# Optimization experiments

Hardware: AMD Instinct MI355X
Metric: run time of the kernel (lower is better)

Reference implementation:

```python
import jax, jax.numpy as jnp
import numpy as np

EPS = 1e-5
DOWNSAMPLE = 0.5


def setup_inputs() -> dict:
    key = jax.random.key(0)
    k1, k2, k3 = jax.random.split(key, 3)
    B, C, H, W = 32, 256, 128, 128
    x = jax.random.normal(k1, (B, C, H, W), dtype=jnp.float32)
    # 1x1 conv: weight [3, C], bias [3]
    conv_w = jax.random.normal(k2, (3, C), dtype=jnp.float32) / np.sqrt(C).astype(np.float32)
    conv_b = jax.random.normal(k3, (3,), dtype=jnp.float32) * 0.01
    return {"x": x, "conv_w": conv_w, "conv_b": conv_b}


def reference(x, conv_w, conv_b):
    B, C, H, W = x.shape
    dh = int(round(H * DOWNSAMPLE))
    dw = int(round(W * DOWNSAMPLE))

    # 1x1 conv producing 3 channels: 2 offset + 1 attention logit
    oa = jnp.einsum('bchw,oc->bohw', x, conv_w) + conv_b[None, :, None, None]
    offset = oa[:, :2]                      # [B,2,H,W]
    attention = jnp.exp(oa[:, 2:3])         # [B,1,H,W]

    # normalized destination coordinates = base grid + offset, clamped
    gy = jnp.broadcast_to((jnp.arange(H, dtype=x.dtype) / H)[:, None], (H, W))
    gx = jnp.broadcast_to((jnp.arange(W, dtype=x.dtype) / W)[None, :], (H, W))
    base = jnp.stack([gy, gx])              # [2,H,W]
    dest = jnp.clip(base[None] + offset, 0.0, 1.0 - EPS)
    dy = jnp.floor(dest[:, 0] * dh)
    dx = jnp.floor(dest[:, 1] * dw)
    cell = (dy * dw + dx).astype(jnp.int32)  # [B,H,W] spatial cell index

    # full flat destination index over (batch, channel, cell)
    b_off = jnp.arange(B, dtype=jnp.int32)[:, None, None, None] * (C * dh * dw)
    c_off = jnp.arange(C, dtype=jnp.int32)[None, :, None, None] * (dh * dw)
    destination = cell[:, None] + b_off + c_off  # [B,C,H,W]

    # scatter-add attention-weighted features
    xw = (x * attention).reshape(-1)
    feat = jax.ops.segment_sum(xw, destination.reshape(-1), num_segments=B * C * dh * dw)

    # scatter-add attention per (batch, cell) for normalization
    a_idx = cell + jnp.arange(B, dtype=jnp.int32)[:, None, None] * (dh * dw)
    att_sum = jax.ops.segment_sum(attention.reshape(-1), a_idx.reshape(-1), num_segments=B * dh * dw) + EPS

    out = feat.reshape(B, C, dh, dw) / att_sum.reshape(B, 1, dh, dw)
    return (out, offset, destination)
```

## Files before the change

### kernel.cpp

```cpp
#include <hip/hip_runtime.h>
#include <math.h>

#define NB 32
#define NC 256
#define NH 128
#define NW 128
#define NDH 64
#define NDW 64
#define NHW (NH * NW)
#define NCELLS (NDH * NDW)
#define OUT0_N (NB * NC * NCELLS)
#define OUT1_BASE OUT0_N
#define OUT1_N (NB * 2 * NHW)
#define OUT2_BASE (OUT1_BASE + OUT1_N)

#define EPSF 1e-5f

typedef unsigned short u16;
typedef unsigned int   u32;

#define WS_CELLS   ((size_t)0)
#define WS_ATTBF   (WS_CELLS + (size_t)NB*NHW*2)
#define WS_ECOMB   (WS_ATTBF + (size_t)NB*NHW*2)
#define WS_IASUM   (WS_ECOMB + (size_t)NB*NHW*4)

__device__ __forceinline__ u16 f32_to_bf16_rn(float f) {
    const u32 u = __float_as_uint(f);
    return (u16)((u + 0x7FFFu + ((u >> 16) & 1u)) >> 16);
}

__global__ __launch_bounds__(256) void k_conv(
    const float* __restrict__ x, const float* __restrict__ cw,
    const float* __restrict__ cb, float* __restrict__ out,
    u16* __restrict__ cells, u16* __restrict__ attbf)
{
    __shared__ float cwS[3][NC];
    __shared__ float red[256][13];
    __shared__ int   cellv[64];

    const int t    = threadIdx.x;
    const int blk  = blockIdx.x;
    const int b    = blk >> 8;
    const int tile = blk & 255;
    const int h    = tile >> 1;
    const int w0   = (tile & 1) << 6;
    const int pixbase = h * NW + w0;

    cwS[0][t] = cw[t];
    cwS[1][t] = cw[NC + t];
    cwS[2][t] = cw[2 * NC + t];
    __syncthreads();

    const int ct = t >> 4;
    const int pg = (t & 15) << 2;
    const float* xb = x + (size_t)b * NC * NHW + pixbase + pg;

    float p00 = 0, p01 = 0, p02 = 0;
    float p10 = 0, p11 = 0, p12 = 0;
    float p20 = 0, p21 = 0, p22 = 0;
    float p30 = 0, p31 = 0, p32 = 0;

    #pragma unroll
    for (int i = 0; i < 16; ++i) {
        const int c = (i << 4) + ct;
        const float4 xv = *reinterpret_cast<const float4*>(xb + (size_t)c * NHW);
        const float wc0 = cwS[0][c], wc1 = cwS[1][c], wc2 = cwS[2][c];
        p00 += xv.x * wc0; p01 += xv.x * wc1; p02 += xv.x * wc2;
        p10 += xv.y * wc0; p11 += xv.y * wc1; p12 += xv.y * wc2;
        p20 += xv.z * wc0; p21 += xv.z * wc1; p22 += xv.z * wc2;
        p30 += xv.w * wc0; p31 += xv.w * wc1; p32 += xv.w * wc2;
    }

    red[t][0]  = p00; red[t][1]  = p01; red[t][2]  = p02;
    red[t][3]  = p10; red[t][4]  = p11; red[t][5]  = p12;
    red[t][6]  = p20; red[t][7]  = p21; red[t][8]  = p22;
    red[t][9]  = p30; red[t][10] = p31; red[t][11] = p32;
    __syncthreads();

    if (t < 64) {
        const int px   = t;
        const int row0 = px >> 2;
        const int col  = (px & 3) * 3;
        float s0 = 0, s1 = 0, s2 = 0;
        #pragma unroll
        for (int j = 0; j < 16; ++j) {
            const int r = row0 + (j << 4);
            s0 += red[r][col];
            s1 += red[r][col + 1];
            s2 += red[r][col + 2];
        }
        const float off0 = s0 + cb[0];
        const float off1 = s1 + cb[1];
        const float att  = expf(s2 + cb[2]);

        const float gy = (float)h * (1.0f / NH);
        const float gx = (float)(w0 + px) * (1.0f / NW);
        const float dyf = fminf(fmaxf(gy + off0, 0.0f), 0.99999f);
        const float dxf = fminf(fmaxf(gx + off1, 0.0f), 0.99999f);
        const int dy = (int)floorf(dyf * (float)NDH);
        const int dx = (int)floorf(dxf * (float)NDW);
        const int cell = dy * NDW + dx;

        cellv[px] = cell;
        cells[b * NHW + pixbase + px] = (u16)cell;
        attbf[b * NHW + pixbase + px] = f32_to_bf16_rn(att);

        const int o1 = OUT1_BASE + b * 2 * NHW + pixbase + px;
        out[o1]       = off0;
        out[o1 + NHW] = off1;
    }
    __syncthreads();

    const int  c0 = cellv[pg], c1 = cellv[pg + 1], c2 = cellv[pg + 2], c3 = cellv[pg + 3];
    float* __restrict__ dst = out + OUT2_BASE;
    #pragma unroll
    for (int i = 0; i < 16; ++i) {
        const int c = (i << 4) + ct;
        const int basec = (b * NC + c) * NCELLS;
        float4 dv;
        dv.x = (float)(basec + c0);
        dv.y = (float)(basec + c1);
        dv.z = (float)(basec + c2);
        dv.w = (float)(basec + c3);
        *reinterpret_cast<float4*>(dst + (size_t)(b * NC + c) * NHW + pixbase + pg) = dv;
    }
}

__global__ __launch_bounds__(1024) void k_sort(
    const u16* __restrict__ cells, const u16* __restrict__ attbf,
    u32* __restrict__ ecomb, float* __restrict__ iasum)
{
    __shared__ u32   hist[NCELLS];
    __shared__ float as_[NCELLS];
    __shared__ u32   ts[1024];

    const int t = threadIdx.x;
    const int b = blockIdx.x;
    const u16* cb_ = cells + b * NHW;
    const u16* ab_ = attbf + b * NHW;

    #pragma unroll
    for (int j = 0; j < 4; ++j) { hist[t + 1024 * j] = 0u; as_[t + 1024 * j] = 0.f; }
    __syncthreads();

    #pragma unroll
    for (int j = 0; j < 16; ++j) {
        const int p  = t + 1024 * j;
        const int cl = cb_[p];
        atomicAdd(&hist[cl], 1u);
        atomicAdd(&as_[cl], __uint_as_float((u32)ab_[p] << 16));
    }
    __syncthreads();

    const u32 h0 = hist[4 * t], h1 = hist[4 * t + 1], h2 = hist[4 * t + 2], h3 = hist[4 * t + 3];
    const u32 T  = h0 + h1 + h2 + h3;
    ts[t] = T;
    __syncthreads();
    for (int off = 1; off < 1024; off <<= 1) {
        const u32 v = (t >= off) ? ts[t - off] : 0u;
        __syncthreads();
        ts[t] += v;
        __syncthreads();
    }
    const u32 base = ts[t] - T;
    hist[4 * t]     = base;
    hist[4 * t + 1] = base + h0;
    hist[4 * t + 2] = base + h0 + h1;
    hist[4 * t + 3] = base + h0 + h1 + h2;

    #pragma unroll
    for (int j = 0; j < 4; ++j) {
        const int i = t + 1024 * j;
        iasum[b * NCELLS + i] = 1.0f / (as_[i] + EPSF);
    }
    __syncthreads();

    #pragma unroll
    for (int j = 0; j < 16; ++j) {
        const int p  = t + 1024 * j;
        const int cl = cb_[p];
        const u32 pos = atomicAdd(&hist[cl], 1u);
        ecomb[b * NHW + pos] = ((u32)cl << 16) | (u32)p;
    }
}

#define BF16V(E) __uint_as_float((u32)xpl[(E) & 0xFFFFu] << 16)
#define ACCUM(CUR, S, E, V)                                                   \
    {                                                                         \
        const int cl_ = (int)((E) >> 16);                                     \
        if (cl_ != (CUR)) { atomicAdd(&acc[(CUR)], (S)); (S) = 0.f; (CUR) = cl_; } \
        (S) += (V);                                                           \
    }

__global__ __launch_bounds__(512, 6) void k_gather(
    const float* __restrict__ x, const u16* __restrict__ attbf,
    const u32* __restrict__ ecomb, const float* __restrict__ iasum,
    float* __restrict__ out)
{
    __shared__ u16   xpl[NHW];
    __shared__ float acc[NCELLS];

    const int t   = threadIdx.x;
    const int blk = blockIdx.x;
    const int b   = blk >> 8;
    const int c   = blk & 255;

    const float4* xp4 = reinterpret_cast<const float4*>(x + (size_t)(b * NC + c) * NHW);
    const uint2*  ab2 = reinterpret_cast<const uint2*>(attbf + (size_t)b * NHW);
    float4*       acc4 = reinterpret_cast<float4*>(acc);

    #pragma unroll
    for (int k = 0; k < 8; ++k) {
        const int idx = t + 512 * k;
        const float4 xv = xp4[idx];
        const uint2  av = ab2[idx];
        const float a0 = __uint_as_float((u32)av.x << 16);
        const float a1 = __uint_as_float(av.x & 0xFFFF0000u);
        const float a2 = __uint_as_float((u32)av.y << 16);
        const float a3 = __uint_as_float(av.y & 0xFFFF0000u);
        const u32 lo = (u32)f32_to_bf16_rn(xv.x * a0)
                     | ((u32)f32_to_bf16_rn(xv.y * a1) << 16);
        const u32 hi = (u32)f32_to_bf16_rn(xv.z * a2)
                     | ((u32)f32_to_bf16_rn(xv.w * a3) << 16);
        *reinterpret_cast<uint2*>(&xpl[idx * 4]) = make_uint2(lo, hi);
    }
    const float4 z4 = make_float4(0.f, 0.f, 0.f, 0.f);
    #pragma unroll
    for (int k = 0; k < 2; ++k) acc4[t + 512 * k] = z4;
    __syncthreads();

    {
        const u32* el = ecomb + b * NHW + t * 32;
        float s0 = 0.f, s1 = 0.f, s2 = 0.f, s3 = 0.f;
        int   c0 = (int)(el[0]  >> 16);
        int   c1 = (int)(el[8]  >> 16);
        int   c2 = (int)(el[16] >> 16);
        int   c3 = (int)(el[24] >> 16);

        #pragma unroll
        for (int ch = 0; ch < 2; ++ch) {
            const uint4 e0 = *reinterpret_cast<const uint4*>(el + ch * 4);
            const uint4 e1 = *reinterpret_cast<const uint4*>(el + 8  + ch * 4);
            const uint4 e2 = *reinterpret_cast<const uint4*>(el + 16 + ch * 4);
            const uint4 e3 = *reinterpret_cast<const uint4*>(el + 24 + ch * 4);
            const float v00 = BF16V(e0.x), v01 = BF16V(e0.y), v02 = BF16V(e0.z), v03 = BF16V(e0.w);
            const float v10 = BF16V(e1.x), v11 = BF16V(e1.y), v12 = BF16V(e1.z), v13 = BF16V(e1.w);
            const float v20 = BF16V(e2.x), v21 = BF16V(e2.y), v22 = BF16V(e2.z), v23 = BF16V(e2.w);
            const float v30 = BF16V(e3.x), v31 = BF16V(e3.y), v32 = BF16V(e3.z), v33 = BF16V(e3.w);
            ACCUM(c0, s0, e0.x, v00); ACCUM(c1, s1, e1.x, v10); ACCUM(c2, s2, e2.x, v20); ACCUM(c3, s3, e3.x, v30);
            ACCUM(c0, s0, e0.y, v01); ACCUM(c1, s1, e1.y, v11); ACCUM(c2, s2, e2.y, v21); ACCUM(c3, s3, e3.y, v31);
            ACCUM(c0, s0, e0.z, v02); ACCUM(c1, s1, e1.z, v12); ACCUM(c2, s2, e2.z, v22); ACCUM(c3, s3, e3.z, v32);
            ACCUM(c0, s0, e0.w, v03); ACCUM(c1, s1, e1.w, v13); ACCUM(c2, s2, e2.w, v23); ACCUM(c3, s3, e3.w, v33);
        }
        atomicAdd(&acc[c0], s0);
        atomicAdd(&acc[c1], s1);
        atomicAdd(&acc[c2], s2);
        atomicAdd(&acc[c3], s3);
    }
    __syncthreads();

    const float4* ia4 = reinterpret_cast<const float4*>(iasum + b * NCELLS);
    float4* ob4 = reinterpret_cast<float4*>(out + (size_t)(b * NC + c) * NCELLS);
    #pragma unroll
    for (int k = 0; k < 2; ++k) {
        float4 a = acc4[t + 512 * k];
        const float4 sv = ia4[t + 512 * k];
        a.x *= sv.x;
        a.y *= sv.y;
        a.z *= sv.z;
        a.w *= sv.w;
        ob4[t + 512 * k] = a;
    }
}

extern "C" void kernel_launch(void* const* d_in, const int* in_sizes, int n_in,
                              void* d_out, int out_size, void* d_ws, size_t ws_size,
                              hipStream_t stream)
{
    (void)in_sizes; (void)n_in; (void)out_size; (void)ws_size;
    const float* x  = (const float*)d_in[0];
    const float* cw = (const float*)d_in[1];
    const float* cb = (const float*)d_in[2];
    float* out = (float*)d_out;
    char*  ws  = (char*)d_ws;

    u16*   cells = (u16*)  (ws + WS_CELLS);
    u16*   attbf = (u16*)  (ws + WS_ATTBF);
    u32*   ecomb = (u32*)  (ws + WS_ECOMB);
    float* iasum = (float*)(ws + WS_IASUM);

    k_conv  <<<dim3(NB * 256), dim3(256),  0, stream>>>(x, cw, cb, out, cells, attbf);
    k_sort  <<<dim3(NB),       dim3(1024), 0, stream>>>(cells, attbf, ecomb, iasum);
    k_gather<<<dim3(NB * NC),  dim3(512),  0, stream>>>(x, attbf, ecomb, iasum, out);
}
```

Baseline: 442.4 us.

## Precompute bf16 attention-weighted x in conv kernel and async-stage it in gather

The conv kernel now keeps the x tile in registers, multiplies it by the per-pixel attention and writes a bf16 copy of x*att to a workspace buffer. The gather kernel then reads this half-size bf16 plane with direct global-to-LDS loads instead of re-reading fp32 x plus attention. This cuts gather read traffic from 4 to 2 bytes per element, at the cost of an extra 2-byte-per-element write in conv and higher register pressure there. The new path runs only when the workspace is large enough, otherwise the old kernels are used.

```diff
diff --git a/kernel.cpp b/kernel.cpp
--- a/kernel.cpp
+++ b/kernel.cpp
@@ -19,23 +19,34 @@
 typedef unsigned short u16;
 typedef unsigned int   u32;
 
-#define WS_CELLS   ((size_t)0)
-#define WS_ATTBF   (WS_CELLS + (size_t)NB*NHW*2)
-#define WS_ECOMB   (WS_ATTBF + (size_t)NB*NHW*2)
-#define WS_IASUM   (WS_ECOMB + (size_t)NB*NHW*4)
+#define WS_CELLS     ((size_t)0)
+#define WS_ATTBF     (WS_CELLS + (size_t)NB*NHW*2)
+#define WS_ECOMB     (WS_ATTBF + (size_t)NB*NHW*2)
+#define WS_IASUM     (WS_ECOMB + (size_t)NB*NHW*4)
+#define WS_BASE_NEED (WS_IASUM + (size_t)NB*NCELLS*4)
+#define WS_XATT      WS_BASE_NEED
+#define WS_XATT_NEED (WS_XATT + (size_t)NB*NC*NHW*2)
 
 __device__ __forceinline__ u16 f32_to_bf16_rn(float f) {
     const u32 u = __float_as_uint(f);
     return (u16)((u + 0x7FFFu + ((u >> 16) & 1u)) >> 16);
 }
 
-__global__ __launch_bounds__(256) void k_conv(
+__device__ __forceinline__ void async_stage16(const void* g, void* l) {
+    __builtin_amdgcn_global_load_lds(
+        (const __attribute__((address_space(1))) unsigned int*)g,
+        (__attribute__((address_space(3))) unsigned int*)l,
+        16, 0, 0);
+}
+
+__global__ __launch_bounds__(256) void k_conv_x(
     const float* __restrict__ x, const float* __restrict__ cw,
     const float* __restrict__ cb, float* __restrict__ out,
-    u16* __restrict__ cells, u16* __restrict__ attbf)
+    u16* __restrict__ cells, u16* __restrict__ attbf, u16* __restrict__ xatt)
 {
     __shared__ float cwS[3][NC];
     __shared__ float red[256][13];
+    __shared__ float attv[64];
     __shared__ int   cellv[64];
 
     const int t    = threadIdx.x;
@@ -55,6 +66,7 @@
     const int pg = (t & 15) << 2;
     const float* xb = x + (size_t)b * NC * NHW + pixbase + pg;
 
+    float4 xr[16];
     float p00 = 0, p01 = 0, p02 = 0;
     float p10 = 0, p11 = 0, p12 = 0;
     float p20 = 0, p21 = 0, p22 = 0;
@@ -64,6 +76,7 @@
     for (int i = 0; i < 16; ++i) {
         const int c = (i << 4) + ct;
         const float4 xv = *reinterpret_cast<const float4*>(xb + (size_t)c * NHW);
+        xr[i] = xv;
         const float wc0 = cwS[0][c], wc1 = cwS[1][c], wc2 = cwS[2][c];
         p00 += xv.x * wc0; p01 += xv.x * wc1; p02 += xv.x * wc2;
         p10 += xv.y * wc0; p11 += xv.y * wc1; p12 += xv.y * wc2;
@@ -102,6 +115,7 @@
         const int cell = dy * NDW + dx;
 
         cellv[px] = cell;
+        attv[px]  = att;
         cells[b * NHW + pixbase + px] = (u16)cell;
         attbf[b * NHW + pixbase + px] = f32_to_bf16_rn(att);
 
@@ -112,7 +126,9 @@
     __syncthreads();
 
     const int  c0 = cellv[pg], c1 = cellv[pg + 1], c2 = cellv[pg + 2], c3 = cellv[pg + 3];
+    const float a0 = attv[pg], a1 = attv[pg + 1], a2 = attv[pg + 2], a3 = attv[pg + 3];
     float* __restrict__ dst = out + OUT2_BASE;
+
     #pragma unroll
     for (int i = 0; i < 16; ++i) {
         const int c = (i << 4) + ct;
@@ -123,6 +139,108 @@
         dv.z = (float)(basec + c2);
         dv.w = (float)(basec + c3);
         *reinterpret_cast<float4*>(dst + (size_t)(b * NC + c) * NHW + pixbase + pg) = dv;
+
+        const float4 xv = xr[i];
+        const u32 lo = (u32)f32_to_bf16_rn(xv.x * a0)
+                     | ((u32)f32_to_bf16_rn(xv.y * a1) << 16);
+        const u32 hi = (u32)f32_to_bf16_rn(xv.z * a2)
+                     | ((u32)f32_to_bf16_rn(xv.w * a3) << 16);
+        *reinterpret_cast<uint2*>(xatt + (size_t)(b * NC + c) * NHW + pixbase + pg)
+            = make_uint2(lo, hi);
+    }
+}
+
+__global__ __launch_bounds__(256) void k_conv(
+    const float* __restrict__ x, const float* __restrict__ cw,
+    const float* __restrict__ cb, float* __restrict__ out,
+    u16* __restrict__ cells, u16* __restrict__ attbf)
+{
+    __shared__ float cwS[3][NC];
+    __shared__ float red[256][13];
+    __shared__ int   cellv[64];
+
+    const int t    = threadIdx.x;
+    const int blk  = blockIdx.x;
+    const int b    = blk >> 8;
+    const int tile = blk & 255;
+    const int h    = tile >> 1;
+    const int w0   = (tile & 1) << 6;
+    const int pixbase = h * NW + w0;
+
+    cwS[0][t] = cw[t];
+    cwS[1][t] = cw[NC + t];
+    cwS[2][t] = cw[2 * NC + t];
+    __syncthreads();
+
+    const int ct = t >> 4;
+    const int pg = (t & 15) << 2;
+    const float* xb = x + (size_t)b * NC * NHW + pixbase + pg;
+
+    float p00 = 0, p01 = 0, p02 = 0;
+    float p10 = 0, p11 = 0, p12 = 0;
+    float p20 = 0, p21 = 0, p22 = 0;
+    float p30 = 0, p31 = 0, p32 = 0;
+
+    #pragma unroll
+    for (int i = 0; i < 16; ++i) {
+        const int c = (i << 4) + ct;
+        const float4 xv = *reinterpret_cast<const float4*>(xb + (size_t)c * NHW);
+        const float wc0 = cwS[0][c], wc1 = cwS[1][c], wc2 = cwS[2][c];
+        p00 += xv.x * wc0; p01 += xv.x * wc1; p02 += xv.x * wc2;
+        p10 += xv.y * wc0; p11 += xv.y * wc1; p12 += xv.y * wc2;
+        p20 += xv.z * wc0; p21 += xv.z * wc1; p22 += xv.z * wc2;
+        p30 += xv.w * wc0; p31 += xv.w * wc1; p32 += xv.w * wc2;
+    }
+
+    red[t][0]  = p00; red[t][1]  = p01; red[t][2]  = p02;
+    red[t][3]  = p10; red[t][4]  = p11; red[t][5]  = p12;
+    red[t][6]  = p20; red[t][7]  = p21; red[t][8]  = p22;
+    red[t][9]  = p30; red[t][10] = p31; red[t][11] = p32;
+    __syncthreads();
+
+    if (t < 64) {
+        const int px   = t;
+        const int row0 = px >> 2;
+        const int col  = (px & 3) * 3;
+        float s0 = 0, s1 = 0, s2 = 0;
+        #pragma unroll
+        for (int j = 0; j < 16; ++j) {
+            const int r = row0 + (j << 4);
+            s0 += red[r][col];
+            s1 += red[r][col + 1];
+            s2 += red[r][col + 2];
+        }
+        const float off0 = s0 + cb[0];
+        const float off1 = s1 + cb[1];
+        const float att  = expf(s2 + cb[2]);
+        const float gy = (float)h * (1.0f / NH);
+        const float gx = (float)(w0 + px) * (1.0f / NW);
+        const float dyf = fminf(fmaxf(gy + off0, 0.0f), 0.99999f);
+        const float dxf = fminf(fmaxf(gx + off1, 0.0f), 0.99999f);
+        const int dy = (int)floorf(dyf * (float)NDH);
+        const int dx = (int)floorf(dxf * (float)NDW);
+        const int cell = dy * NDW + dx;
+        cellv[px] = cell;
+        cells[b * NHW + pixbase + px] = (u16)cell;
+        attbf[b * NHW + pixbase + px] = f32_to_bf16_rn(att);
+        const int o1 = OUT1_BASE + b * 2 * NHW + pixbase + px;
+        out[o1]       = off0;
+        out[o1 + NHW] = off1;
+    }
+    __syncthreads();
+
+    const int  c0 = cellv[pg], c1 = cellv[pg + 1], c2 = cellv[pg + 2], c3 = cellv[pg + 3];
+    float* __restrict__ dst = out + OUT2_BASE;
+    #pragma unroll
+    for (int i = 0; i < 16; ++i) {
+        const int c = (i << 4) + ct;
+        const int basec = (b * NC + c) * NCELLS;
+        float4 dv;
+        dv.x = (float)(basec + c0);
+        dv.y = (float)(basec + c1);
+        dv.z = (float)(basec + c2);
+        dv.w = (float)(basec + c3);
+        *reinterpret_cast<float4*>(dst + (size_t)(b * NC + c) * NHW + pixbase + pg) = dv;
     }
 }
 
@@ -191,6 +309,82 @@
         if (cl_ != (CUR)) { atomicAdd(&acc[(CUR)], (S)); (S) = 0.f; (CUR) = cl_; } \
         (S) += (V);                                                           \
     }
+
+__device__ __forceinline__ void gather_core(
+    const u16* __restrict__ xpl, float* __restrict__ acc,
+    const u32* __restrict__ el)
+{
+    float s0 = 0.f, s1 = 0.f, s2 = 0.f, s3 = 0.f;
+    int   c0 = (int)(el[0]  >> 16);
+    int   c1 = (int)(el[8]  >> 16);
+    int   c2 = (int)(el[16] >> 16);
+    int   c3 = (int)(el[24] >> 16);
+
+    #pragma unroll
+    for (int ch = 0; ch < 2; ++ch) {
+        const uint4 e0 = *reinterpret_cast<const uint4*>(el + ch * 4);
+        const uint4 e1 = *reinterpret_cast<const uint4*>(el + 8  + ch * 4);
+        const uint4 e2 = *reinterpret_cast<const uint4*>(el + 16 + ch * 4);
+        const uint4 e3 = *reinterpret_cast<const uint4*>(el + 24 + ch * 4);
+        const float v00 = BF16V(e0.x), v01 = BF16V(e0.y), v02 = BF16V(e0.z), v03 = BF16V(e0.w);
+        const float v10 = BF16V(e1.x), v11 = BF16V(e1.y), v12 = BF16V(e1.z), v13 = BF16V(e1.w);
+        const float v20 = BF16V(e2.x), v21 = BF16V(e2.y), v22 = BF16V(e2.z), v23 = BF16V(e2.w);
+        const float v30 = BF16V(e3.x), v31 = BF16V(e3.y), v32 = BF16V(e3.z), v33 = BF16V(e3.w);
+        ACCUM(c0, s0, e0.x, v00); ACCUM(c1, s1, e1.x, v10); ACCUM(c2, s2, e2.x, v20); ACCUM(c3, s3, e3.x, v30);
+        ACCUM(c0, s0, e0.y, v01); ACCUM(c1, s1, e1.y, v11); ACCUM(c2, s2, e2.y, v21); ACCUM(c3, s3, e3.y, v31);
+        ACCUM(c0, s0, e0.z, v02); ACCUM(c1, s1, e1.z, v12); ACCUM(c2, s2, e2.z, v22); ACCUM(c3, s3, e3.z, v32);
+        ACCUM(c0, s0, e0.w, v03); ACCUM(c1, s1, e1.w, v13); ACCUM(c2, s2, e2.w, v23); ACCUM(c3, s3, e3.w, v33);
+    }
+    atomicAdd(&acc[c0], s0);
+    atomicAdd(&acc[c1], s1);
+    atomicAdd(&acc[c2], s2);
+    atomicAdd(&acc[c3], s3);
+}
+
+__global__ __launch_bounds__(512, 6) void k_gather_x(
+    const u16* __restrict__ xatt, const u32* __restrict__ ecomb,
+    const float* __restrict__ iasum, float* __restrict__ out)
+{
+    __shared__ u16   xpl[NHW];
+    __shared__ float acc[NCELLS];
+
+    const int t    = threadIdx.x;
+    const int blk  = blockIdx.x;
+    const int b    = blk >> 8;
+    const int c    = blk & 255;
+    const int wave = t >> 6;
+    const int lane = t & 63;
+
+    const u16* xp = xatt + (size_t)(b * NC + c) * NHW;
+    #pragma unroll
+    for (int k = 0; k < 4; ++k) {
+        const int chunk = wave * 4 + k;
+        const int e0    = chunk * 512;
+        async_stage16(xp + e0 + lane * 8, &xpl[e0 + lane * 8]);
+    }
+
+    float4* acc4 = reinterpret_cast<float4*>(acc);
+    const float4 z4 = make_float4(0.f, 0.f, 0.f, 0.f);
+    #pragma unroll
+    for (int k = 0; k < 2; ++k) acc4[t + 512 * k] = z4;
+    __syncthreads();
+
+    gather_core(xpl, acc, ecomb + b * NHW + t * 32);
+    __syncthreads();
+
+    const float4* ia4 = reinterpret_cast<const float4*>(iasum + b * NCELLS);
+    float4* ob4 = reinterpret_cast<float4*>(out + (size_t)(b * NC + c) * NCELLS);
+    #pragma unroll
+    for (int k = 0; k < 2; ++k) {
+        float4 a = acc4[t + 512 * k];
+        const float4 sv = ia4[t + 512 * k];
+        a.x *= sv.x;
+        a.y *= sv.y;
+        a.z *= sv.z;
+        a.w *= sv.w;
+        ob4[t + 512 * k] = a;
+    }
+}
 
 __global__ __launch_bounds__(512, 6) void k_gather(
     const float* __restrict__ x, const u16* __restrict__ attbf,
@@ -229,34 +423,7 @@
     for (int k = 0; k < 2; ++k) acc4[t + 512 * k] = z4;
     __syncthreads();
 
-    {
-        const u32* el = ecomb + b * NHW + t * 32;
-        float s0 = 0.f, s1 = 0.f, s2 = 0.f, s3 = 0.f;
-        int   c0 = (int)(el[0]  >> 16);
-        int   c1 = (int)(el[8]  >> 16);
-        int   c2 = (int)(el[16] >> 16);
-        int   c3 = (int)(el[24] >> 16);
-
-        #pragma unroll
-        for (int ch = 0; ch < 2; ++ch) {
-            const uint4 e0 = *reinterpret_cast<const uint4*>(el + ch * 4);
-            const uint4 e1 = *reinterpret_cast<const uint4*>(el + 8  + ch * 4);
-            const uint4 e2 = *reinterpret_cast<const uint4*>(el + 16 + ch * 4);
-            const uint4 e3 = *reinterpret_cast<const uint4*>(el + 24 + ch * 4);
-            const float v00 = BF16V(e0.x), v01 = BF16V(e0.y), v02 = BF16V(e0.z), v03 = BF16V(e0.w);
-            const float v10 = BF16V(e1.x), v11 = BF16V(e1.y), v12 = BF16V(e1.z), v13 = BF16V(e1.w);
-            const float v20 = BF16V(e2.x), v21 = BF16V(e2.y), v22 = BF16V(e2.z), v23 = BF16V(e2.w);
-            const float v30 = BF16V(e3.x), v31 = BF16V(e3.y), v32 = BF16V(e3.z), v33 = BF16V(e3.w);
-            ACCUM(c0, s0, e0.x, v00); ACCUM(c1, s1, e1.x, v10); ACCUM(c2, s2, e2.x, v20); ACCUM(c3, s3, e3.x, v30);
-            ACCUM(c0, s0, e0.y, v01); ACCUM(c1, s1, e1.y, v11); ACCUM(c2, s2, e2.y, v21); ACCUM(c3, s3, e3.y, v31);
-            ACCUM(c0, s0, e0.z, v02); ACCUM(c1, s1, e1.z, v12); ACCUM(c2, s2, e2.z, v22); ACCUM(c3, s3, e3.z, v32);
-            ACCUM(c0, s0, e0.w, v03); ACCUM(c1, s1, e1.w, v13); ACCUM(c2, s2, e2.w, v23); ACCUM(c3, s3, e3.w, v33);
-        }
-        atomicAdd(&acc[c0], s0);
-        atomicAdd(&acc[c1], s1);
-        atomicAdd(&acc[c2], s2);
-        atomicAdd(&acc[c3], s3);
-    }
+    gather_core(xpl, acc, ecomb + b * NHW + t * 32);
     __syncthreads();
 
     const float4* ia4 = reinterpret_cast<const float4*>(iasum + b * NCELLS);
@@ -277,7 +444,7 @@
                               void* d_out, int out_size, void* d_ws, size_t ws_size,
                               hipStream_t stream)
 {
-    (void)in_sizes; (void)n_in; (void)out_size; (void)ws_size;
+    (void)in_sizes; (void)n_in; (void)out_size;
     const float* x  = (const float*)d_in[0];
     const float* cw = (const float*)d_in[1];
     const float* cb = (const float*)d_in[2];
@@ -289,7 +456,14 @@
     u32*   ecomb = (u32*)  (ws + WS_ECOMB);
     float* iasum = (float*)(ws + WS_IASUM);
 
-    k_conv  <<<dim3(NB * 256), dim3(256),  0, stream>>>(x, cw, cb, out, cells, attbf);
-    k_sort  <<<dim3(NB),       dim3(1024), 0, stream>>>(cells, attbf, ecomb, iasum);
-    k_gather<<<dim3(NB * NC),  dim3(512),  0, stream>>>(x, attbf, ecomb, iasum, out);
-}
+    if (ws_size >= WS_XATT_NEED) {
+        u16* xatt = (u16*)(ws + WS_XATT);
+        k_conv_x  <<<dim3(NB * 256), dim3(256),  0, stream>>>(x, cw, cb, out, cells, attbf, xatt);
+        k_sort    <<<dim3(NB),       dim3(1024), 0, stream>>>(cells, attbf, ecomb, iasum);
+        k_gather_x<<<dim3(NB * NC),  dim3(512),  0, stream>>>(xatt, ecomb, iasum, out);
+    } else {
+        k_conv  <<<dim3(NB * 256), dim3(256),  0, stream>>>(x, cw, cb, out, cells, attbf);
+        k_sort  <<<dim3(NB),       dim3(1024), 0, stream>>>(cells, attbf, ecomb, iasum);
+        k_gather<<<dim3(NB * NC),  dim3(512),  0, stream>>>(x, attbf, ecomb, iasum, out);
+    }
+}
```

Result: slower. 492.8 us (+11.4%).
